# Kernel optimization log

Measured on AMD Instinct MI355X. Metric: run time of the kernel, lower is better.

Reference implementation:

```python
import jax, jax.numpy as jnp
import numpy as np

NUM_EXPERTS = 8


def setup_inputs() -> dict:
    key = jax.random.key(0)
    ks = jax.random.split(key, 5)
    B, S, H, F, E = 4, 2048, 1024, 4096, NUM_EXPERTS
    scale_h = 1.0 / np.sqrt(H)
    scale_f = 1.0 / np.sqrt(F)
    return {
        "x": jax.random.normal(ks[0], (B, S, H), jnp.float32),
        "router_w": jax.random.normal(ks[1], (H, E), jnp.float32) * scale_h,
        "router_b": jnp.zeros((E,), jnp.float32),
        "w1": jax.random.normal(ks[2], (E, H, F), jnp.float32) * scale_h,
        "b1": jnp.zeros((E, F), jnp.float32),
        "w2": jax.random.normal(ks[3], (E, F, H), jnp.float32) * scale_f,
        "b2": jnp.zeros((E, H), jnp.float32),
        "top_k": 2,
    }


def reference(x, router_w, router_b, w1, b1, w2, b2, top_k):
    B, S, H = x.shape
    E = w1.shape[0]
    xf = x.reshape(B * S, H)                              # [T, H]
    logits = xf @ router_w + router_b                     # [T, E]
    probs = jax.nn.softmax(logits, axis=-1)
    topw, topi = jax.lax.top_k(probs, top_k)              # [T, k]
    topw = topw / jnp.sum(topw, axis=-1, keepdims=True)
    # per-token combine weight for each expert (0 if not selected) [T, E]
    comb = jnp.sum(jax.nn.one_hot(topi, E, dtype=xf.dtype) * topw[..., None], axis=1)
    out = jnp.zeros_like(xf)
    for e in range(E):  # fixed small loop over experts
        h = jax.nn.gelu(xf @ w1[e] + b1[e])               # [T, F]
        y = h @ w2[e] + b2[e]                             # [T, H]
        out = out + comb[:, e:e + 1] * y
    return out.reshape(B, S, H)
```

## Files before the change

### kernel.cpp

```cpp
#include <hip/hip_runtime.h>
#include <cstdint>

#define TOKENS 8192
#define H_DIM  1024
#define F_DIM  4096
#define E_NUM  8
#define ASSIGN (TOKENS * 2)
#define MAXSEG 144

using short8 = __attribute__((ext_vector_type(8))) short;
using f32x4  = __attribute__((ext_vector_type(4))) float;

__device__ __forceinline__ unsigned short f32_to_bf16(float f) {
  unsigned int u = __float_as_uint(f);
  u += 0x7FFFu + ((u >> 16) & 1u);
  return (unsigned short)(u >> 16);
}

__device__ __forceinline__ void direct_load16(const void* g, void* l) {
  __builtin_amdgcn_global_load_lds(
      (const __attribute__((address_space(1))) unsigned int*)(uintptr_t)g,
      (__attribute__((address_space(3))) unsigned int*)(uintptr_t)l,
      16, 0, 0);
}

__device__ __forceinline__ void transpose_tile(
    const float* __restrict__ src, unsigned short* __restrict__ dst,
    int R, int C, int e, int bx, int by, int tid) {
  __shared__ unsigned short t[64][68];
  size_t base = (size_t)e * R * C;
  int c0 = bx * 64, r0 = by * 64;
  int rl = tid >> 4, c4 = (tid & 15) * 4;
#pragma unroll
  for (int i = 0; i < 4; ++i) {
    int r = rl + 16 * i;
    float4 v = *(const float4*)(src + base + (size_t)(r0 + r) * C + c0 + c4);
    t[c4 + 0][r] = f32_to_bf16(v.x);
    t[c4 + 1][r] = f32_to_bf16(v.y);
    t[c4 + 2][r] = f32_to_bf16(v.z);
    t[c4 + 3][r] = f32_to_bf16(v.w);
  }
  __syncthreads();
  int cc = tid >> 3, rr = (tid & 7) * 8;
#pragma unroll
  for (int i = 0; i < 2; ++i) {
    int c = cc + 32 * i;
#pragma unroll
    for (int j = 0; j < 2; ++j) {
      ushort4 v = *(const ushort4*)&t[c][rr + 4 * j];
      *(ushort4*)(dst + base + (size_t)(c0 + c) * R + r0 + rr + 4 * j) = v;
    }
  }
}

__global__ __launch_bounds__(256) void prep_kernel(
    const float* __restrict__ x, const float* __restrict__ w1, const float* __restrict__ w2,
    const float* __restrict__ rw, const float* __restrict__ rb,
    unsigned short* __restrict__ xb, unsigned short* __restrict__ w1t,
    unsigned short* __restrict__ w2t,
    int2* __restrict__ tok_e, float2* __restrict__ tok_w) {
  int id = blockIdx.x, tid = threadIdx.x;
  if (id < 8192) {
    int i = id * 256 + tid;
    float4 v = ((const float4*)x)[i];
    ushort4 o;
    o.x = f32_to_bf16(v.x); o.y = f32_to_bf16(v.y);
    o.z = f32_to_bf16(v.z); o.w = f32_to_bf16(v.w);
    ((ushort4*)xb)[i] = o;
  } else if (id < 16384) {
    int lo = id - 8192;
    transpose_tile(w1, w1t, H_DIM, F_DIM, lo >> 10, (lo & 1023) & 63, (lo & 1023) >> 6, tid);
  } else if (id < 24576) {
    int lo = id - 16384;
    transpose_tile(w2, w2t, F_DIM, H_DIM, lo >> 10, (lo & 1023) & 15, (lo & 1023) >> 4, tid);
  } else {
    int t = (id - 24576) * 4 + (tid >> 6);
    int lane = tid & 63;
    float acc[8];
#pragma unroll
    for (int e = 0; e < 8; ++e) acc[e] = 0.f;
    const float* xr = x + (long)t * H_DIM;
#pragma unroll 4
    for (int j = 0; j < H_DIM / 64; ++j) {
      int hh = lane + 64 * j;
      float xv = xr[hh];
      const float4* w4 = (const float4*)(rw + (long)hh * 8);
      float4 wa = w4[0], wb = w4[1];
      acc[0] += xv * wa.x; acc[1] += xv * wa.y; acc[2] += xv * wa.z; acc[3] += xv * wa.w;
      acc[4] += xv * wb.x; acc[5] += xv * wb.y; acc[6] += xv * wb.z; acc[7] += xv * wb.w;
    }
#pragma unroll
    for (int e = 0; e < 8; ++e) {
      float v = acc[e];
      for (int off = 32; off > 0; off >>= 1) v += __shfl_xor(v, off, 64);
      acc[e] = v + rb[e];
    }
    if (lane == 0) {
      int e0 = 0; float l0 = acc[0];
#pragma unroll
      for (int e = 1; e < 8; ++e) if (acc[e] > l0) { l0 = acc[e]; e0 = e; }
      int e1 = -1; float l1 = -3.4e38f;
#pragma unroll
      for (int e = 0; e < 8; ++e) if (e != e0 && acc[e] > l1) { l1 = acc[e]; e1 = e; }
      float w0 = 1.f / (1.f + expf(l1 - l0));
      tok_e[t] = make_int2(e0, e1);
      tok_w[t] = make_float2(w0, 1.f - w0);
    }
  }
}

__global__ __launch_bounds__(256) void hist_kernel(
    const int2* __restrict__ tok_e, int* __restrict__ ctrl) {
  __shared__ int lc[8];
  int tid = threadIdx.x;
  if (tid < 8) lc[tid] = 0;
  __syncthreads();
  int2 e = tok_e[blockIdx.x * 256 + tid];
  atomicAdd(&lc[e.x], 1);
  atomicAdd(&lc[e.y], 1);
  __syncthreads();
  if (tid < 8) ctrl[512 + blockIdx.x * 8 + tid] = lc[tid];
}

__global__ void plan_kernel(int* __restrict__ ctrl) {
  int lane = threadIdx.x;
  if (lane < 8) {
    int run = 0;
    for (int b = 0; b < 32; ++b) {
      ctrl[768 + b * 8 + lane] = run;
      run += ctrl[512 + b * 8 + lane];
    }
    ctrl[lane] = run;
  }
  __syncthreads();
  if (lane == 0) {
    int run = 0, ns = 0;
    ctrl[8] = 0;
    for (int e = 0; e < 8; ++e) {
      int cnt = ctrl[e];
      run += cnt;
      ctrl[9 + e] = run;
      for (int r0 = 0; r0 < cnt; r0 += 128) { ctrl[32 + ns] = e; ctrl[256 + ns] = r0; ++ns; }
    }
    ctrl[25] = ns;
  }
  __syncthreads();
  if (lane < 8) {
    int off = ctrl[8 + lane];
    for (int b = 0; b < 32; ++b) ctrl[768 + b * 8 + lane] += off;
  }
}

__global__ __launch_bounds__(256) void place_kernel(
    const int2* __restrict__ tok_e, const float2* __restrict__ tok_w,
    const int* __restrict__ ctrl, int* __restrict__ atok, float* __restrict__ aw) {
  __shared__ int lc[8];
  int tid = threadIdx.x;
  if (tid < 8) lc[tid] = 0;
  __syncthreads();
  int t = blockIdx.x * 256 + tid;
  int2 e = tok_e[t];
  float2 wv = tok_w[t];
  int l0 = atomicAdd(&lc[e.x], 1);
  int l1 = atomicAdd(&lc[e.y], 1);
  int p0 = ctrl[768 + blockIdx.x * 8 + e.x] + l0;
  int p1 = ctrl[768 + blockIdx.x * 8 + e.y] + l1;
  atok[p0] = t; aw[p0] = wv.x;
  atok[p1] = t; aw[p1] = wv.y;
}

template <int K, int NTOT, bool PHASE2>
__global__ __launch_bounds__(256, 4) void moe_gemm_kernel(
    const unsigned short* __restrict__ Abase,
    const unsigned short* __restrict__ Bbase,
    const float* __restrict__ bias,
    const int* __restrict__ ctrl,
    const int* __restrict__ atok,
    const float* __restrict__ aw,
    unsigned short* __restrict__ Hout,
    float* __restrict__ Out) {
  const int seg = blockIdx.y;
  if (seg >= ctrl[25]) return;
  const int e = ctrl[32 + seg];
  const int row0 = ctrl[256 + seg];
  const int off_e = ctrl[8 + e];
  const int Ne = ctrl[9 + e] - off_e;
  const int n0 = blockIdx.x * 128;

  __shared__ __align__(16) unsigned short As[128 * 64];
  __shared__ __align__(16) unsigned short Bs[128 * 64];

  const int tid = threadIdx.x;
  const int lane = tid & 63;
  const int w = tid >> 6;
  const int wm = w >> 1, wn = w & 1;

  const int lrow = lane >> 3;
  const int q = (lane & 7) ^ lrow;

  unsigned int goff[8];
#pragma unroll
  for (int j = 0; j < 8; ++j) {
    int t = w * 8 + j;
    if (t < 16) {
      int r = row0 + t * 8 + lrow;
      if (r > Ne - 1) r = Ne - 1;
      unsigned int srow = PHASE2 ? (unsigned int)(off_e + r) : (unsigned int)atok[off_e + r];
      goff[j] = srow * (unsigned int)K + q * 8;
    } else {
      int brow = (t - 16) * 8 + lrow;
      goff[j] = (unsigned int)((size_t)e * NTOT * K + (size_t)(n0 + brow) * K) + q * 8;
    }
  }

  const int quad = lane >> 4, l15 = lane & 15, l7 = lane & 7;

  f32x4 acc[4][4];
#pragma unroll
  for (int i = 0; i < 4; ++i)
#pragma unroll
    for (int j = 0; j < 4; ++j) acc[i][j] = f32x4{0.f, 0.f, 0.f, 0.f};

  for (int k0 = 0; k0 < K; k0 += 64) {
    __syncthreads();
#pragma unroll
    for (int j = 0; j < 8; ++j) {
      int t = w * 8 + j;
      unsigned short* dst = (t < 16) ? &As[t * 512] : &Bs[(t - 16) * 512];
      const unsigned short* src = (t < 16) ? Abase : Bbase;
      direct_load16(src + goff[j] + k0, dst);
    }
    __syncthreads();
#pragma unroll
    for (int ks = 0; ks < 2; ++ks) {
      short8 af[4], bfr[4];
      const int c = ((ks * 4 + quad) ^ l7) * 8;
#pragma unroll
      for (int i = 0; i < 4; ++i)
        af[i] = *(const short8*)&As[(wm * 64 + i * 16 + l15) * 64 + c];
#pragma unroll
      for (int j = 0; j < 4; ++j)
        bfr[j] = *(const short8*)&Bs[(wn * 64 + j * 16 + l15) * 64 + c];
#pragma unroll
      for (int i = 0; i < 4; ++i)
#pragma unroll
        for (int j = 0; j < 4; ++j)
          acc[i][j] = __builtin_amdgcn_mfma_f32_16x16x32_bf16(af[i], bfr[j], acc[i][j], 0, 0, 0);
    }
  }

#pragma unroll
  for (int j = 0; j < 4; ++j) {
    int gn = n0 + wn * 64 + j * 16 + l15;
    float bv = bias[(size_t)e * NTOT + gn];
#pragma unroll
    for (int i = 0; i < 4; ++i) {
      int gmb = row0 + wm * 64 + i * 16 + quad * 4;
#pragma unroll
      for (int r = 0; r < 4; ++r) {
        int gm = gmb + r;
        if (gm < Ne) {
          float v = acc[i][j][r] + bv;
          if (!PHASE2) {
            float ex = __expf(-1.5957691216057308f * (v + 0.044715f * v * v * v));
            float g = v * __builtin_amdgcn_rcpf(1.f + ex);
            Hout[(size_t)(off_e + gm) * NTOT + gn] = f32_to_bf16(g);
          } else {
            int tok = atok[off_e + gm];
            float wt = aw[off_e + gm];
            atomicAdd(Out + (size_t)tok * NTOT + gn, v * wt);
          }
        }
      }
    }
  }
}

extern "C" void kernel_launch(void* const* d_in, const int* in_sizes, int n_in,
                              void* d_out, int out_size, void* d_ws, size_t ws_size,
                              hipStream_t stream) {
  const float* x  = (const float*)d_in[0];
  const float* rw = (const float*)d_in[1];
  const float* rb = (const float*)d_in[2];
  const float* w1 = (const float*)d_in[3];
  const float* b1 = (const float*)d_in[4];
  const float* w2 = (const float*)d_in[5];
  const float* b2 = (const float*)d_in[6];
  float* out = (float*)d_out;

  char* ws = (char*)d_ws;
  size_t off = 0;
  auto take = [&](size_t b) { char* p = ws + off; off = (off + b + 255) & ~(size_t)255; return p; };
  unsigned short* xb   = (unsigned short*)take((size_t)TOKENS * H_DIM * 2);
  unsigned short* w1t  = (unsigned short*)take((size_t)E_NUM * F_DIM * H_DIM * 2);
  unsigned short* w2t  = (unsigned short*)take((size_t)E_NUM * H_DIM * F_DIM * 2);
  unsigned short* hbuf = (unsigned short*)take((size_t)ASSIGN * F_DIM * 2);
  int2*   tok_e = (int2*)take(TOKENS * sizeof(int2));
  float2* tok_w = (float2*)take(TOKENS * sizeof(float2));
  int*    atok  = (int*)take(ASSIGN * 4);
  float*  aw    = (float*)take(ASSIGN * 4);
  int*    ctrl  = (int*)take(4096);

  hipMemsetAsync(out, 0, (size_t)out_size * 4, stream);

  prep_kernel<<<26624, 256, 0, stream>>>(x, w1, w2, rw, rb, xb, w1t, w2t, tok_e, tok_w);
  hist_kernel<<<TOKENS / 256, 256, 0, stream>>>(tok_e, ctrl);
  plan_kernel<<<1, 64, 0, stream>>>(ctrl);
  place_kernel<<<TOKENS / 256, 256, 0, stream>>>(tok_e, tok_w, ctrl, atok, aw);
  moe_gemm_kernel<H_DIM, F_DIM, false><<<dim3(F_DIM / 128, MAXSEG), 256, 0, stream>>>(
      xb, w1t, b1, ctrl, atok, aw, hbuf, nullptr);
  moe_gemm_kernel<F_DIM, H_DIM, true><<<dim3(H_DIM / 128, MAXSEG), 256, 0, stream>>>(
      hbuf, w2t, b2, ctrl, atok, aw, nullptr, out);
}
```

Measured before the change: 843.8 us.

## Use persistent stream-K scheduling for second expert GEMM and fuse router into cast

The second expert GEMM moves from a fixed grid over (n-tile, segment) to a persistent grid of 1024 blocks. Each block takes a balanced contiguous range of (tile, k-chunk) work and accumulates partial sums into the output with atomics, adding bias only on the first k-chunk. This targets tail imbalance and idle blocks from the padded segment grid, at the cost of more atomic traffic when a tile's K range is split across blocks. The router logits are also folded into the x-to-bf16 conversion blocks, so x is read once and the separate router blocks go away.

```diff
diff --git a/kernel.cpp b/kernel.cpp
--- a/kernel.cpp
+++ b/kernel.cpp
@@ -7,6 +7,7 @@
 #define E_NUM  8
 #define ASSIGN (TOKENS * 2)
 #define MAXSEG 144
+#define GEMM2_W 1024
 
 using short8 = __attribute__((ext_vector_type(8))) short;
 using f32x4  = __attribute__((ext_vector_type(4))) float;
@@ -59,53 +60,56 @@
     unsigned short* __restrict__ xb, unsigned short* __restrict__ w1t,
     unsigned short* __restrict__ w2t,
     int2* __restrict__ tok_e, float2* __restrict__ tok_w) {
+  __shared__ float rsum[4][8];
   int id = blockIdx.x, tid = threadIdx.x;
   if (id < 8192) {
-    int i = id * 256 + tid;
-    float4 v = ((const float4*)x)[i];
+    float4 v = ((const float4*)x)[id * 256 + tid];
     ushort4 o;
     o.x = f32_to_bf16(v.x); o.y = f32_to_bf16(v.y);
     o.z = f32_to_bf16(v.z); o.w = f32_to_bf16(v.w);
-    ((ushort4*)xb)[i] = o;
+    ((ushort4*)xb)[id * 256 + tid] = o;
+    float p[8];
+#pragma unroll
+    for (int e = 0; e < 8; ++e) p[e] = 0.f;
+    const float4* w4 = (const float4*)(rw + (size_t)tid * 32);
+    float xv;
+#pragma unroll
+    for (int j = 0; j < 4; ++j) {
+      xv = (j == 0) ? v.x : (j == 1) ? v.y : (j == 2) ? v.z : v.w;
+      float4 wa = w4[j * 2], wb = w4[j * 2 + 1];
+      p[0] += xv * wa.x; p[1] += xv * wa.y; p[2] += xv * wa.z; p[3] += xv * wa.w;
+      p[4] += xv * wb.x; p[5] += xv * wb.y; p[6] += xv * wb.z; p[7] += xv * wb.w;
+    }
+#pragma unroll
+    for (int e = 0; e < 8; ++e)
+      for (int off = 32; off > 0; off >>= 1) p[e] += __shfl_xor(p[e], off, 64);
+    int wv = tid >> 6, lane = tid & 63;
+    if (lane == 0) {
+#pragma unroll
+      for (int e = 0; e < 8; ++e) rsum[wv][e] = p[e];
+    }
+    __syncthreads();
+    if (tid == 0) {
+      float a[8];
+#pragma unroll
+      for (int e = 0; e < 8; ++e)
+        a[e] = rsum[0][e] + rsum[1][e] + rsum[2][e] + rsum[3][e] + rb[e];
+      int e0 = 0; float l0 = a[0];
+#pragma unroll
+      for (int e = 1; e < 8; ++e) if (a[e] > l0) { l0 = a[e]; e0 = e; }
+      int e1 = -1; float l1 = -3.4e38f;
+#pragma unroll
+      for (int e = 0; e < 8; ++e) if (e != e0 && a[e] > l1) { l1 = a[e]; e1 = e; }
+      float w0 = 1.f / (1.f + expf(l1 - l0));
+      tok_e[id] = make_int2(e0, e1);
+      tok_w[id] = make_float2(w0, 1.f - w0);
+    }
   } else if (id < 16384) {
     int lo = id - 8192;
     transpose_tile(w1, w1t, H_DIM, F_DIM, lo >> 10, (lo & 1023) & 63, (lo & 1023) >> 6, tid);
-  } else if (id < 24576) {
+  } else {
     int lo = id - 16384;
     transpose_tile(w2, w2t, F_DIM, H_DIM, lo >> 10, (lo & 1023) & 15, (lo & 1023) >> 4, tid);
-  } else {
-    int t = (id - 24576) * 4 + (tid >> 6);
-    int lane = tid & 63;
-    float acc[8];
-#pragma unroll
-    for (int e = 0; e < 8; ++e) acc[e] = 0.f;
-    const float* xr = x + (long)t * H_DIM;
-#pragma unroll 4
-    for (int j = 0; j < H_DIM / 64; ++j) {
-      int hh = lane + 64 * j;
-      float xv = xr[hh];
-      const float4* w4 = (const float4*)(rw + (long)hh * 8);
-      float4 wa = w4[0], wb = w4[1];
-      acc[0] += xv * wa.x; acc[1] += xv * wa.y; acc[2] += xv * wa.z; acc[3] += xv * wa.w;
-      acc[4] += xv * wb.x; acc[5] += xv * wb.y; acc[6] += xv * wb.z; acc[7] += xv * wb.w;
-    }
-#pragma unroll
-    for (int e = 0; e < 8; ++e) {
-      float v = acc[e];
-      for (int off = 32; off > 0; off >>= 1) v += __shfl_xor(v, off, 64);
-      acc[e] = v + rb[e];
-    }
-    if (lane == 0) {
-      int e0 = 0; float l0 = acc[0];
-#pragma unroll
-      for (int e = 1; e < 8; ++e) if (acc[e] > l0) { l0 = acc[e]; e0 = e; }
-      int e1 = -1; float l1 = -3.4e38f;
-#pragma unroll
-      for (int e = 0; e < 8; ++e) if (e != e0 && acc[e] > l1) { l1 = acc[e]; e1 = e; }
-      float w0 = 1.f / (1.f + expf(l1 - l0));
-      tok_e[t] = make_int2(e0, e1);
-      tok_w[t] = make_float2(w0, 1.f - w0);
-    }
   }
 }
 
@@ -169,16 +173,15 @@
   atok[p1] = t; aw[p1] = wv.y;
 }
 
-template <int K, int NTOT, bool PHASE2>
-__global__ __launch_bounds__(256, 4) void moe_gemm_kernel(
+
+template <int K, int NTOT>
+__global__ __launch_bounds__(256, 4) void moe_gemm1_kernel(
     const unsigned short* __restrict__ Abase,
     const unsigned short* __restrict__ Bbase,
     const float* __restrict__ bias,
     const int* __restrict__ ctrl,
     const int* __restrict__ atok,
-    const float* __restrict__ aw,
-    unsigned short* __restrict__ Hout,
-    float* __restrict__ Out) {
+    unsigned short* __restrict__ Hout) {
   const int seg = blockIdx.y;
   if (seg >= ctrl[25]) return;
   const int e = ctrl[32 + seg];
@@ -194,7 +197,6 @@
   const int lane = tid & 63;
   const int w = tid >> 6;
   const int wm = w >> 1, wn = w & 1;
-
   const int lrow = lane >> 3;
   const int q = (lane & 7) ^ lrow;
 
@@ -205,8 +207,7 @@
     if (t < 16) {
       int r = row0 + t * 8 + lrow;
       if (r > Ne - 1) r = Ne - 1;
-      unsigned int srow = PHASE2 ? (unsigned int)(off_e + r) : (unsigned int)atok[off_e + r];
-      goff[j] = srow * (unsigned int)K + q * 8;
+      goff[j] = (unsigned int)atok[off_e + r] * (unsigned int)K + q * 8;
     } else {
       int brow = (t - 16) * 8 + lrow;
       goff[j] = (unsigned int)((size_t)e * NTOT * K + (size_t)(n0 + brow) * K) + q * 8;
@@ -261,11 +262,120 @@
         int gm = gmb + r;
         if (gm < Ne) {
           float v = acc[i][j][r] + bv;
-          if (!PHASE2) {
-            float ex = __expf(-1.5957691216057308f * (v + 0.044715f * v * v * v));
-            float g = v * __builtin_amdgcn_rcpf(1.f + ex);
-            Hout[(size_t)(off_e + gm) * NTOT + gn] = f32_to_bf16(g);
-          } else {
+          float ex = __expf(-1.5957691216057308f * (v + 0.044715f * v * v * v));
+          float g = v * __builtin_amdgcn_rcpf(1.f + ex);
+          Hout[(size_t)(off_e + gm) * NTOT + gn] = f32_to_bf16(g);
+        }
+      }
+    }
+  }
+}
+
+template <int K, int NTOT>
+__global__ __launch_bounds__(256, 4) void moe_gemm2_kernel(
+    const unsigned short* __restrict__ Abase,
+    const unsigned short* __restrict__ Bbase,
+    const float* __restrict__ bias,
+    const int* __restrict__ ctrl,
+    const int* __restrict__ atok,
+    const float* __restrict__ aw,
+    float* __restrict__ Out) {
+  constexpr int NX  = NTOT / 128;
+  constexpr int GPI = K / 64;
+  const int nseg = ctrl[25];
+  const int G = nseg * NX * GPI;
+  const int W = (int)gridDim.x;
+  const int qg = G / W, rg = G % W;
+  const int b = (int)blockIdx.x;
+  int g0   = b * qg + (b < rg ? b : rg);
+  int gend = g0 + qg + (b < rg ? 1 : 0);
+
+  __shared__ __align__(16) unsigned short As[128 * 64];
+  __shared__ __align__(16) unsigned short Bs[128 * 64];
+
+  const int tid = threadIdx.x;
+  const int lane = tid & 63;
+  const int w = tid >> 6;
+  const int wm = w >> 1, wn = w & 1;
+  const int lrow = lane >> 3;
+  const int qc = (lane & 7) ^ lrow;
+  const int quad = lane >> 4, l15 = lane & 15, l7 = lane & 7;
+
+  while (g0 < gend) {
+    const int item = g0 / GPI;
+    const int ko   = g0 - item * GPI;
+    int glen = gend - g0;
+    if (glen > GPI - ko) glen = GPI - ko;
+
+    const int seg = item / NX;
+    const int x   = item - seg * NX;
+    const int e = ctrl[32 + seg];
+    const int row0 = ctrl[256 + seg];
+    const int off_e = ctrl[8 + e];
+    const int Ne = ctrl[9 + e] - off_e;
+    const int n0 = x * 128;
+
+    unsigned int goff[8];
+#pragma unroll
+    for (int j = 0; j < 8; ++j) {
+      int t = w * 8 + j;
+      if (t < 16) {
+        int r = row0 + t * 8 + lrow;
+        if (r > Ne - 1) r = Ne - 1;
+        goff[j] = (unsigned int)(off_e + r) * (unsigned int)K + qc * 8;
+      } else {
+        int brow = (t - 16) * 8 + lrow;
+        goff[j] = (unsigned int)((size_t)e * NTOT * K + (size_t)(n0 + brow) * K) + qc * 8;
+      }
+    }
+
+    f32x4 acc[4][4];
+#pragma unroll
+    for (int i = 0; i < 4; ++i)
+#pragma unroll
+      for (int j = 0; j < 4; ++j) acc[i][j] = f32x4{0.f, 0.f, 0.f, 0.f};
+
+    for (int kk = 0; kk < glen; ++kk) {
+      const int k0 = (ko + kk) * 64;
+      __syncthreads();
+#pragma unroll
+      for (int j = 0; j < 8; ++j) {
+        int t = w * 8 + j;
+        unsigned short* dst = (t < 16) ? &As[t * 512] : &Bs[(t - 16) * 512];
+        const unsigned short* src = (t < 16) ? Abase : Bbase;
+        direct_load16(src + goff[j] + k0, dst);
+      }
+      __syncthreads();
+#pragma unroll
+      for (int ks = 0; ks < 2; ++ks) {
+        short8 af[4], bfr[4];
+        const int c = ((ks * 4 + quad) ^ l7) * 8;
+#pragma unroll
+        for (int i = 0; i < 4; ++i)
+          af[i] = *(const short8*)&As[(wm * 64 + i * 16 + l15) * 64 + c];
+#pragma unroll
+        for (int j = 0; j < 4; ++j)
+          bfr[j] = *(const short8*)&Bs[(wn * 64 + j * 16 + l15) * 64 + c];
+#pragma unroll
+        for (int i = 0; i < 4; ++i)
+#pragma unroll
+          for (int j = 0; j < 4; ++j)
+            acc[i][j] = __builtin_amdgcn_mfma_f32_16x16x32_bf16(af[i], bfr[j], acc[i][j], 0, 0, 0);
+      }
+    }
+
+#pragma unroll
+    for (int j = 0; j < 4; ++j) {
+      int gn = n0 + wn * 64 + j * 16 + l15;
+      float bv = (ko == 0) ? bias[(size_t)e * NTOT + gn] : 0.f;
+#pragma unroll
+      for (int i = 0; i < 4; ++i) {
+        int gmb = row0 + wm * 64 + i * 16 + quad * 4;
+#pragma unroll
+        for (int r = 0; r < 4; ++r) {
+          int gm = gmb + r;
+          if (gm < Ne) {
+            float v = acc[i][j][r] + bv;
             int tok = atok[off_e + gm];
             float wt = aw[off_e + gm];
             atomicAdd(Out + (size_t)tok * NTOT + gn, v * wt);
@@ -273,6 +383,8 @@
         }
       }
     }
+
+    g0 += glen;
   }
 }
 
@@ -303,12 +415,12 @@
 
   hipMemsetAsync(out, 0, (size_t)out_size * 4, stream);
 
-  prep_kernel<<<26624, 256, 0, stream>>>(x, w1, w2, rw, rb, xb, w1t, w2t, tok_e, tok_w);
+  prep_kernel<<<24576, 256, 0, stream>>>(x, w1, w2, rw, rb, xb, w1t, w2t, tok_e, tok_w);
   hist_kernel<<<TOKENS / 256, 256, 0, stream>>>(tok_e, ctrl);
   plan_kernel<<<1, 64, 0, stream>>>(ctrl);
   place_kernel<<<TOKENS / 256, 256, 0, stream>>>(tok_e, tok_w, ctrl, atok, aw);
-  moe_gemm_kernel<H_DIM, F_DIM, false><<<dim3(F_DIM / 128, MAXSEG), 256, 0, stream>>>(
-      xb, w1t, b1, ctrl, atok, aw, hbuf, nullptr);
-  moe_gemm_kernel<F_DIM, H_DIM, true><<<dim3(H_DIM / 128, MAXSEG), 256, 0, stream>>>(
-      hbuf, w2t, b2, ctrl, atok, aw, nullptr, out);
-}
+  moe_gemm1_kernel<H_DIM, F_DIM><<<dim3(F_DIM / 128, MAXSEG), 256, 0, stream>>>(
+      xb, w1t, b1, ctrl, atok, hbuf);
+  moe_gemm2_kernel<F_DIM, H_DIM><<<GEMM2_W, 256, 0, stream>>>(
+      hbuf, w2t, b2, ctrl, atok, aw, out);
+}
```

Result: slower. 948.6 us (+12.4%).
